# Performance work log

Hardware: AMD Instinct MI355X
Metric: run time of the kernel (lower is better)

The kernel has to match this reference:

```python
import jax, jax.numpy as jnp
import numpy as np
import math

H, KVH, D = 15, 5, 64  # heads, kv heads, head_dim
ROPE_BASE = 10000.0
NEG = -1e9


def _rope_cos_sin(position_ids):
    # position_ids: [B, S] int -> cos/sin [B, 1, S, D]
    inv_freq = 1.0 / (ROPE_BASE ** (jnp.arange(0, D, 2, dtype=jnp.float32) / D))  # [D/2]
    freqs = position_ids.astype(jnp.float32)[..., None] * inv_freq  # [B, S, D/2]
    emb = jnp.concatenate([freqs, freqs], axis=-1)  # [B, S, D]
    return jnp.cos(emb)[:, None], jnp.sin(emb)[:, None]


def _rotate_half(x):
    x1, x2 = x[..., : D // 2], x[..., D // 2 :]
    return jnp.concatenate([-x2, x1], axis=-1)


def setup_inputs() -> dict:
    key = jax.random.key(0)
    ks = jax.random.split(key, 5)
    B, S, E = 1, 4096, 960
    hidden_states = jax.random.normal(ks[0], (B, S, E), dtype=jnp.float32)
    Wq = jax.random.normal(ks[1], (E, E), dtype=jnp.float32) * 0.02
    Wk = jax.random.normal(ks[2], (KVH * D, E), dtype=jnp.float32) * 0.02
    Wv = jax.random.normal(ks[3], (KVH * D, E), dtype=jnp.float32) * 0.02
    Wo = jax.random.normal(ks[4], (E, E), dtype=jnp.float32) * 0.02
    causal = jnp.tril(jnp.ones((S, S), dtype=bool))
    attention_mask = jnp.where(causal, 0.0, NEG).astype(jnp.float32)[None, None]  # [1,1,S,S]
    position_ids = jnp.arange(S, dtype=jnp.int64 if jax.config.jax_enable_x64 else jnp.int32)[None]
    return {
        "hidden_states": hidden_states,
        "Wq": Wq,
        "Wk": Wk,
        "Wv": Wv,
        "Wo": Wo,
        "attention_mask": attention_mask,
        "position_ids": position_ids,
    }


def reference(hidden_states, Wq, Wk, Wv, Wo, attention_mask, position_ids):
    B, S, E = hidden_states.shape
    groups = H // KVH
    # projections (bias-free Linear: x @ W.T)
    q = (hidden_states @ Wq.T).reshape(B, S, H, D).transpose(0, 2, 1, 3)      # [B,H,S,D]
    k = (hidden_states @ Wk.T).reshape(B, S, KVH, D).transpose(0, 2, 1, 3)    # [B,KVH,S,D]
    v = (hidden_states @ Wv.T).reshape(B, S, KVH, D).transpose(0, 2, 1, 3)    # [B,KVH,S,D]
    cos, sin = _rope_cos_sin(position_ids)  # [B,1,S,D]
    q = q * cos + _rotate_half(q) * sin
    k = k * cos + _rotate_half(k) * sin
    # GQA: repeat_interleave over the head axis
    k = jnp.repeat(k, groups, axis=1)  # [B,H,S,D]
    v = jnp.repeat(v, groups, axis=1)  # [B,H,S,D]
    scores = jnp.einsum("bhqd,bhkd->bhqk", q, k) / math.sqrt(D) + attention_mask
    probs = jax.nn.softmax(scores.astype(jnp.float32), axis=-1).astype(q.dtype)
    out = jnp.einsum("bhqk,bhkd->bhqd", probs, v)  # [B,H,S,D]
    out = out.transpose(0, 2, 1, 3).reshape(B, S, E)
    return out @ Wo.T
```

## Files before the change

### kernel.cpp

```cpp
#include <hip/hip_runtime.h>
#include <hip/hip_bf16.h>

typedef __hip_bfloat16 bf16;
typedef short bf16x8 __attribute__((ext_vector_type(8)));
typedef short bf16x4 __attribute__((ext_vector_type(4)));
typedef float f32x4 __attribute__((ext_vector_type(4)));

static constexpr int S_LEN = 4096;
static constexpr int EMB   = 960;
static constexpr int NH    = 15;
static constexpr int NKVH  = 5;
static constexpr int KV_E  = NKVH * 64;

__device__ __forceinline__ float scrub(float x, float lim) {
  return fminf(fmaxf(x, -lim), lim);
}

__device__ __forceinline__ short f2bf(float x) {
  bf16 h = __float2bfloat16(x);
  short s;
  __builtin_memcpy(&s, &h, 2);
  return s;
}

__device__ __forceinline__ void stage16(const bf16* g, bf16* l) {
  __builtin_amdgcn_global_load_lds(
      (const __attribute__((address_space(1))) void*)g,
      (__attribute__((address_space(3))) void*)l, 16, 0, 0);
}

__global__ void cvt5_kernel(const float* s0, const float* s1, const float* s2,
                            const float* s3, const float* s4,
                            bf16* d0, bf16* d1, bf16* d2, bf16* d3, bf16* d4,
                            int e0, int e1, int e2, int e3, int e4) {
  int i = blockIdx.x * blockDim.x + threadIdx.x;
  const float* s;
  bf16* d;
  int base;
  if (i < e0)      { s = s0; d = d0; base = 0;  }
  else if (i < e1) { s = s1; d = d1; base = e0; }
  else if (i < e2) { s = s2; d = d2; base = e1; }
  else if (i < e3) { s = s3; d = d3; base = e2; }
  else if (i < e4) { s = s4; d = d4; base = e3; }
  else return;
  int k = i - base;
  const float4* sp = (const float4*)s + (size_t)k * 2;
  float4 a = sp[0], b = sp[1];
  bf16x8 r;
  r[0] = f2bf(a.x); r[1] = f2bf(a.y); r[2] = f2bf(a.z); r[3] = f2bf(a.w);
  r[4] = f2bf(b.x); r[5] = f2bf(b.y); r[6] = f2bf(b.z); r[7] = f2bf(b.w);
  *(bf16x8*)((short*)d + (size_t)k * 8) = r;
}

__global__ void zero_kernel(float* __restrict__ p, int n4) {
  int i = blockIdx.x * blockDim.x + threadIdx.x;
  if (i < n4) ((float4*)p)[i] = (float4){0.f, 0.f, 0.f, 0.f};
}

template <typename EPI>
__device__ __forceinline__ void gemm_core(
    const bf16* __restrict__ A, const bf16* __restrict__ W,
    int m0, int n0, int K, bf16* At0, bf16* At1, bf16* Bt0, bf16* Bt1,
    EPI&& epilogue) {
  const int lane = threadIdx.x & 63;
  const int wave = threadIdx.x >> 6;
  const int quad = lane >> 4;
  const int c16  = lane & 15;
  const int wm = wave >> 1, wn = wave & 1;
  const int srow = lane >> 2;
  const int sch  = lane & 3;
  const int NIT  = K / 32;
  bf16* At[2] = {At0, At1};
  bf16* Bt[2] = {Bt0, Bt1};

  auto stage = [&](int b, int k0) {
#pragma unroll
    for (int t = 0; t < 2; t++) {
      int j = wave * 2 + t;
      stage16(A + (size_t)(m0 + j * 16 + srow) * K + k0 + sch * 8,
              At[b] + j * 512);
      stage16(W + (size_t)(n0 + j * 16 + srow) * K + k0 + sch * 8,
              Bt[b] + j * 512);
    }
  };

  f32x4 acc[4][4];
#pragma unroll
  for (int i = 0; i < 4; i++)
#pragma unroll
    for (int j = 0; j < 4; j++) acc[i][j] = (f32x4){0.f, 0.f, 0.f, 0.f};

  stage(0, 0);
  __syncthreads();

  for (int it = 0; it < NIT; ++it) {
    if (it + 1 < NIT) stage((it + 1) & 1, (it + 1) * 32);
    const char* ab = (const char*)At[it & 1];
    const char* bb = (const char*)Bt[it & 1];
    bf16x8 af[4], bfr[4];
#pragma unroll
    for (int i = 0; i < 4; i++)
      af[i] = *(const bf16x8*)(ab + (wm * 64 + i * 16 + c16) * 64 + quad * 16);
#pragma unroll
    for (int j = 0; j < 4; j++)
      bfr[j] = *(const bf16x8*)(bb + (wn * 64 + j * 16 + c16) * 64 + quad * 16);
#pragma unroll
    for (int i = 0; i < 4; i++)
#pragma unroll
      for (int j = 0; j < 4; j++)
        acc[i][j] = __builtin_amdgcn_mfma_f32_16x16x32_bf16(af[i], bfr[j],
                                                            acc[i][j], 0, 0, 0);
    __syncthreads();
  }
  epilogue(acc, m0, n0, wm, wn, quad, c16);
}

__global__ __launch_bounds__(256) void gemm_qkv_kernel(
    const bf16* __restrict__ A, const bf16* __restrict__ Wcat,
    bf16* __restrict__ Qb, bf16* __restrict__ Kbf, bf16* __restrict__ VTb,
    int M, int K) {
  __shared__ __align__(16) bf16 At[2][128 * 32];
  __shared__ __align__(16) bf16 Bt[2][128 * 32];
  const int m0 = blockIdx.x * 128;
  const int n0 = blockIdx.y * 128;
  gemm_core(A, Wcat, m0, n0, K, At[0], At[1], Bt[0], Bt[1],
            [&](f32x4 (&acc)[4][4], int m0_, int n0_, int wm, int wn,
                int quad, int c16) {
#pragma unroll
              for (int i = 0; i < 4; i++)
#pragma unroll
                for (int j = 0; j < 4; j++) {
                  int scol = n0_ + wn * 64 + j * 16;
                  if (scol >= 1600) continue;
                  int colg = scol + c16;
                  int row0 = m0_ + wm * 64 + i * 16 + quad * 4;
                  if (scol < 960) {
#pragma unroll
                    for (int r = 0; r < 4; r++)
                      Qb[(size_t)(row0 + r) * EMB + colg] =
                          __float2bfloat16(scrub(acc[i][j][r], 3e4f));
                  } else if (scol < 1280) {
#pragma unroll
                    for (int r = 0; r < 4; r++)
                      Kbf[(size_t)(row0 + r) * KV_E + (colg - 960)] =
                          __float2bfloat16(scrub(acc[i][j][r], 3e4f));
                  } else {
                    bf16x4 v;
#pragma unroll
                    for (int r = 0; r < 4; r++)
                      v[r] = f2bf(scrub(acc[i][j][r], 3e4f));
                    *(bf16x4*)((short*)VTb + (size_t)(colg - 1280) * S_LEN +
                               row0) = v;
                  }
                }
            });
}

__global__ __launch_bounds__(256) void gemm_out_kernel(
    const bf16* __restrict__ A, const bf16* __restrict__ W,
    float* __restrict__ C, int M, int N, int K) {
  __shared__ __align__(16) bf16 At[2][128 * 32];
  __shared__ __align__(16) bf16 Bt[2][128 * 32];
  const int m0 = blockIdx.x * 128;
  const int n0 = blockIdx.y * 128;
  gemm_core(A, W, m0, n0, K, At[0], At[1], Bt[0], Bt[1],
            [&](f32x4 (&acc)[4][4], int m0_, int n0_, int wm, int wn,
                int quad, int c16) {
#pragma unroll
              for (int i = 0; i < 4; i++)
#pragma unroll
                for (int j = 0; j < 4; j++) {
                  int scol = n0_ + wn * 64 + j * 16;
                  if (scol >= EMB) continue;
                  int col = scol + c16;
                  int row0 = m0_ + wm * 64 + i * 16 + quad * 4;
#pragma unroll
                  for (int r = 0; r < 4; r++)
                    C[(size_t)(row0 + r) * EMB + col] =
                        scrub(acc[i][j][r], 3e4f);
                }
            });
}

__global__ void rope2_kernel(bf16* __restrict__ Qb, bf16* __restrict__ Kb,
                             const int* __restrict__ pos_ids) {
  int tid = blockIdx.x * blockDim.x + threadIdx.x;
  if (tid >= S_LEN * (NH + NKVH) * 32) return;
  int d  = tid & 31;
  int hh = (tid >> 5) % (NH + NKVH);
  int s  = tid / ((NH + NKVH) * 32);
  bf16* buf;
  size_t idx;
  float scale;
  if (hh < NH) {
    buf = Qb; idx = (size_t)s * EMB + hh * 64 + d; scale = 0.125f;
  } else {
    buf = Kb; idx = (size_t)s * KV_E + (hh - NH) * 64 + d; scale = 1.0f;
  }
  float x = __bfloat162float(buf[idx]);
  float y = __bfloat162float(buf[idx + 32]);
  float f = (float)pos_ids[s] * expf((float)d * -0.28782313662425572f);
  float sf, cf;
  sincosf(f, &sf, &cf);
  buf[idx]      = __float2bfloat16(scrub((x * cf - y * sf) * scale, 3e4f));
  buf[idx + 32] = __float2bfloat16(scrub((y * cf + x * sf) * scale, 3e4f));
}

__global__ __launch_bounds__(256, 5) void flash_kernel(
    const bf16* __restrict__ Q, const bf16* __restrict__ Kb,
    const bf16* __restrict__ VT, float* __restrict__ Oacc,
    float* __restrict__ Lacc) {
  __shared__ __align__(16) bf16 Kt[2][64 * 64];
  __shared__ __align__(16) bf16 Vt[2][64 * 64];

  const int xq = (int)(gridDim.x - 1) - (int)blockIdx.x;
  const int c  = blockIdx.z;
  if (c > (xq >> 4)) return;

  const int lane = threadIdx.x & 63;
  const int wv   = threadIdx.x >> 6;
  const int quad = lane >> 4;
  const int c16  = lane & 15;
  const int h    = blockIdx.y;
  const int kvh  = h / 3;
  const int qb   = xq * 64;
  const int qw   = qb + wv * 16;
  const int qcol = qw + c16;
  const int it0   = c * 16;
  const int itend = min(it0 + 16, xq + 1);

  const int rsub = lane >> 3;
  const int gch  = (lane & 7) ^ rsub;
  const int rm   = c16 & 7;
  const int ko0  = (quad ^ rm) * 16;
  const int qh   = quad >> 1;
  const int vsub = (quad & 1) * 8;

  const bf16* qrow = Q + (size_t)qcol * EMB + h * 64 + quad * 8;
  const bf16x8 aq0 = *(const bf16x8*)qrow;
  const bf16x8 aq1 = *(const bf16x8*)(qrow + 32);

  f32x4 o[4];
#pragma unroll
  for (int n = 0; n < 4; n++) o[n] = (f32x4){0.f, 0.f, 0.f, 0.f};
  float osum = 0.f;

  auto stage = [&](int b, int it) {
    const int kbase = it * 64;
#pragma unroll
    for (int t = 0; t < 2; t++) {
      int i = wv * 2 + t;
      int r = i * 8 + rsub;
      stage16(Kb + (size_t)(kbase + r) * KV_E + kvh * 64 + gch * 8,
              &Kt[b][i * 512]);
      stage16(VT + (size_t)(kvh * 64 + r) * S_LEN + kbase + gch * 8,
              &Vt[b][i * 512]);
    }
  };

  stage(0, it0);
  __syncthreads();

  for (int it = it0; it < itend; ++it) {
    if (it + 1 < itend) stage((it + 1) & 1, it + 1);

    const int kbase = it * 64;
    const char* kb = (const char*)&Kt[it & 1][0];
    const char* vb = (const char*)&Vt[it & 1][0];
    const bool masked = (it == xq);

    bf16x4 pp[4];
#pragma unroll
    for (int cc = 0; cc < 4; cc++) {
      int r = cc * 16 + c16;
      bf16x8 b0 = *(const bf16x8*)(kb + r * 128 + ko0);
      bf16x8 b1 = *(const bf16x8*)(kb + r * 128 + (ko0 ^ 64));
      f32x4 s = (f32x4){0.f, 0.f, 0.f, 0.f};
      s = __builtin_amdgcn_mfma_f32_16x16x32_bf16(b0, aq0, s, 0, 0, 0);
      s = __builtin_amdgcn_mfma_f32_16x16x32_bf16(b1, aq1, s, 0, 0, 0);
#pragma unroll
      for (int r4 = 0; r4 < 4; r4++) {
        float p = __expf(fminf(s[r4], 80.f));
        if (masked) {
          int kc = kbase + cc * 16 + quad * 4 + r4;
          p = (kc <= qcol) ? p : 0.f;
        }
        osum += p;
        pp[cc][r4] = f2bf(p);
      }
    }

#pragma unroll
    for (int n = 0; n < 4; n++) {
      const char* vrow = vb + (n * 16 + c16) * 128;
#pragma unroll
      for (int cc = 0; cc < 4; cc++) {
        bf16x4 va =
            *(const bf16x4*)(vrow + (((cc * 2 + qh) ^ rm) * 16) + vsub);
        o[n] = __builtin_amdgcn_mfma_f32_16x16x16bf16_1k(va, pp[cc], o[n],
                                                         0, 0, 0);
      }
    }

    __syncthreads();
  }

  osum += __shfl_xor(osum, 16);
  osum += __shfl_xor(osum, 32);
  if (lane < 16)
    atomicAdd(&Lacc[(size_t)(qw + lane) * NH + h], osum);

  float* zone = (float*)((char*)&Kt[0][0] + wv * 1280 * 4);
#pragma unroll
  for (int n = 0; n < 4; n++) {
    *(f32x4*)(zone + c16 * 20 + quad * 4) = o[n];
    asm volatile("s_waitcnt lgkmcnt(0)" ::: "memory");
#pragma unroll
    for (int r = 0; r < 4; r++) {
      float t = zone[(quad * 4 + r) * 20 + c16];
      atomicAdd(&Oacc[(size_t)(qw + quad * 4 + r) * EMB + h * 64 + n * 16 +
                      c16], t);
    }
    asm volatile("" ::: "memory");
  }
}

__global__ void normalize_kernel(const float* __restrict__ Oacc,
                                 const float* __restrict__ Lacc,
                                 bf16* __restrict__ O) {
  int i = blockIdx.x * blockDim.x + threadIdx.x;
  if (i >= S_LEN * (EMB / 4)) return;
  int row = i / (EMB / 4);
  int col = (i % (EMB / 4)) * 4;
  int h = col >> 6;
  float l = fmaxf(Lacc[(size_t)row * NH + h], 1e-20f);
  float4 v = *(const float4*)&Oacc[(size_t)row * EMB + col];
  bf16x4 r;
  r[0] = f2bf(scrub(v.x / l, 1e4f));
  r[1] = f2bf(scrub(v.y / l, 1e4f));
  r[2] = f2bf(scrub(v.z / l, 1e4f));
  r[3] = f2bf(scrub(v.w / l, 1e4f));
  *(bf16x4*)((short*)O + (size_t)row * EMB + col) = r;
}

extern "C" void kernel_launch(void* const* d_in, const int* in_sizes, int n_in,
                              void* d_out, int out_size, void* d_ws, size_t ws_size,
                              hipStream_t stream) {
  const float* hs = (const float*)d_in[0];
  const float* Wq = (const float*)d_in[1];
  const float* Wk = (const float*)d_in[2];
  const float* Wv = (const float*)d_in[3];
  const float* Wo = (const float*)d_in[4];
  const int* pos = (const int*)d_in[6];
  float* out = (float*)d_out;

  char* wsb = (char*)d_ws;
  float* Oacc = (float*)wsb;
  float* Lacc = Oacc + (size_t)S_LEN * EMB;
  size_t regA = ((size_t)S_LEN * EMB + (size_t)S_LEN * NH) * sizeof(float);
  bf16* hsb = (bf16*)wsb;
  bf16* Qb  = (bf16*)(wsb + regA);
  bf16* Kbf = Qb + (size_t)S_LEN * EMB;
  bf16* VTb = Kbf + (size_t)S_LEN * KV_E;
  bf16* Wqb = VTb + (size_t)S_LEN * KV_E;
  bf16* Wkb = Wqb + (size_t)EMB * EMB;
  bf16* Wvb = Wkb + (size_t)KV_E * EMB;
  bf16* Wob = Wqb + (size_t)1664 * EMB;

  {
    int e0 = (S_LEN * EMB) / 8;
    int e1 = e0 + (EMB * EMB) / 8;
    int e2 = e1 + (KV_E * EMB) / 8;
    int e3 = e2 + (KV_E * EMB) / 8;
    int e4 = e3 + (EMB * EMB) / 8;
    cvt5_kernel<<<(e4 + 255) / 256, 256, 0, stream>>>(
        hs, Wq, Wk, Wv, Wo, hsb, Wqb, Wkb, Wvb, Wob, e0, e1, e2, e3, e4);
  }

  gemm_qkv_kernel<<<dim3(S_LEN / 128, 13), 256, 0, stream>>>(
      hsb, Wqb, Qb, Kbf, VTb, S_LEN, EMB);

  {
    int n = S_LEN * (NH + NKVH) * 32;
    rope2_kernel<<<(n + 255) / 256, 256, 0, stream>>>(Qb, Kbf, pos);
  }

  {
    int n4 = (S_LEN * EMB + S_LEN * NH) / 4;
    zero_kernel<<<(n4 + 255) / 256, 256, 0, stream>>>(Oacc, n4);
  }
  flash_kernel<<<dim3(S_LEN / 64, NH, 4), 256, 0, stream>>>(Qb, Kbf, VTb,
                                                            Oacc, Lacc);
  {
    int n = S_LEN * (EMB / 4);
    normalize_kernel<<<(n + 255) / 256, 256, 0, stream>>>(Oacc, Lacc, Qb);
  }

  gemm_out_kernel<<<dim3(S_LEN / 128, 8), 256, 0, stream>>>(
      Qb, Wob, out, S_LEN, EMB, EMB);
}
```

Measured before the change: 288.0 us.

## Permute V^T token layout for 16-byte LDS reads and compute row sums via MFMA

The QKV projection epilogue now writes V^T with a permuted token order, so each lane in the attention kernel can fetch one bf16x8 from LDS and split it across two MFMAs, instead of issuing two separate bf16x4 reads. The softmax row sum is now accumulated with an MFMA against a vector of ones, replacing the per-element scalar adds and the cross-lane shuffles. The sum is taken over the bf16-rounded probabilities, which matches what the PV product uses. The change adds four extra MFMAs per tile and couples the V layout to the lane mapping inside the attention kernel.

Result: faster. 278.6 us (-3.3%).

```diff
diff --git a/kernel.cpp b/kernel.cpp
--- a/kernel.cpp
+++ b/kernel.cpp
@@ -149,8 +149,10 @@
 #pragma unroll
                     for (int r = 0; r < 4; r++)
                       v[r] = f2bf(scrub(acc[i][j][r], 3e4f));
+                    int t0 = m0_ + wm * 64;
+                    int nl = quad * 16 + (i >> 1) * 8 + (i & 1) * 4;
                     *(bf16x4*)((short*)VTb + (size_t)(colg - 1280) * S_LEN +
-                               row0) = v;
+                               t0 + nl) = v;
                   }
                 }
             });
@@ -233,17 +235,19 @@
   const int gch  = (lane & 7) ^ rsub;
   const int rm   = c16 & 7;
   const int ko0  = (quad ^ rm) * 16;
-  const int qh   = quad >> 1;
-  const int vsub = (quad & 1) * 8;
 
   const bf16* qrow = Q + (size_t)qcol * EMB + h * 64 + quad * 8;
   const bf16x8 aq0 = *(const bf16x8*)qrow;
   const bf16x8 aq1 = *(const bf16x8*)(qrow + 32);
 
+  bf16x4 ones4;
+#pragma unroll
+  for (int j = 0; j < 4; j++) ones4[j] = (short)0x3F80;
+
   f32x4 o[4];
 #pragma unroll
   for (int n = 0; n < 4; n++) o[n] = (f32x4){0.f, 0.f, 0.f, 0.f};
-  float osum = 0.f;
+  f32x4 os = (f32x4){0.f, 0.f, 0.f, 0.f};
 
   auto stage = [&](int b, int it) {
     const int kbase = it * 64;
@@ -285,30 +289,36 @@
           int kc = kbase + cc * 16 + quad * 4 + r4;
           p = (kc <= qcol) ? p : 0.f;
         }
-        osum += p;
         pp[cc][r4] = f2bf(p);
       }
     }
 
 #pragma unroll
+    for (int cc = 0; cc < 4; cc++)
+      os = __builtin_amdgcn_mfma_f32_16x16x16bf16_1k(ones4, pp[cc], os,
+                                                     0, 0, 0);
+
+#pragma unroll
     for (int n = 0; n < 4; n++) {
       const char* vrow = vb + (n * 16 + c16) * 128;
 #pragma unroll
-      for (int cc = 0; cc < 4; cc++) {
-        bf16x4 va =
-            *(const bf16x4*)(vrow + (((cc * 2 + qh) ^ rm) * 16) + vsub);
-        o[n] = __builtin_amdgcn_mfma_f32_16x16x16bf16_1k(va, pp[cc], o[n],
-                                                         0, 0, 0);
+      for (int ccp = 0; ccp < 2; ccp++) {
+        int m = quad * 2 + ccp;
+        bf16x8 vv = *(const bf16x8*)(vrow + ((m ^ rm) * 16));
+        bf16x4 vlo = __builtin_shufflevector(vv, vv, 0, 1, 2, 3);
+        bf16x4 vhi = __builtin_shufflevector(vv, vv, 4, 5, 6, 7);
+        o[n] = __builtin_amdgcn_mfma_f32_16x16x16bf16_1k(vlo, pp[ccp * 2],
+                                                         o[n], 0, 0, 0);
+        o[n] = __builtin_amdgcn_mfma_f32_16x16x16bf16_1k(vhi, pp[ccp * 2 + 1],
+                                                         o[n], 0, 0, 0);
       }
     }
 
     __syncthreads();
   }
 
-  osum += __shfl_xor(osum, 16);
-  osum += __shfl_xor(osum, 32);
-  if (lane < 16)
-    atomicAdd(&Lacc[(size_t)(qw + lane) * NH + h], osum);
+  if (quad == 0)
+    atomicAdd(&Lacc[(size_t)(qw + c16) * NH + h], os[0]);
 
   float* zone = (float*)((char*)&Kt[0][0] + wv * 1280 * 4);
 #pragma unroll
```
